# Kernel tuning notes

Hardware: AMD Instinct MI355X
Metric: run time of the kernel (lower is better)

## Reference

```python
import jax, jax.numpy as jnp
import numpy as np

N = 100000   # nodes
E = 3200000  # edges (avg degree 32)
K = 3        # num_stacks
L = 4        # num_layers (ARMA iterations)
H = 16       # hidden channels
C = 1        # num_classes
BN_EPS = 1e-5


def setup_inputs() -> dict:
    key = jax.random.key(0)
    ks = jax.random.split(key, 16)
    s = 0.1  # weight scale
    return {
        "x": jax.random.normal(ks[0], (N, 1), dtype=jnp.float32),
        "edge_index": jax.random.randint(ks[1], (2, E), 0, N, dtype=jnp.int64),
        "edge_attr": jax.random.uniform(ks[2], (E,), dtype=jnp.float32),
        "batch": jnp.zeros((N,), dtype=jnp.int64),
        # ARMAConv 1: 1 -> 16, shared weights
        "w1_init": s * jax.random.normal(ks[3], (K, 1, H), dtype=jnp.float32),
        "w1": s * jax.random.normal(ks[4], (K, H, H), dtype=jnp.float32),
        "w1_root": s * jax.random.normal(ks[5], (K, 1, H), dtype=jnp.float32),
        "b1": s * jax.random.normal(ks[6], (K, 1, H), dtype=jnp.float32),
        "bn1_g": jnp.ones((H,), dtype=jnp.float32),
        "bn1_b": jnp.zeros((H,), dtype=jnp.float32),
        # ARMAConv 2: 16 -> 1, shared weights, act=None
        "w2_init": s * jax.random.normal(ks[7], (K, H, C), dtype=jnp.float32),
        "w2": s * jax.random.normal(ks[8], (K, C, C), dtype=jnp.float32),
        "w2_root": s * jax.random.normal(ks[9], (K, H, C), dtype=jnp.float32),
        "b2": s * jax.random.normal(ks[10], (K, 1, C), dtype=jnp.float32),
    }


def _arma_conv(x, row, col, norm, w_init, w, w_root, b, n_layers, use_relu):
    """PyG ARMAConv with shared_weights=True, eval-mode dropout (identity).
    x: [N,Fin]; returns mean over K stacks: [N,Fout]."""
    n = x.shape[0]
    root = jnp.einsum('nf,kfo->kno', x, w_root)      # [K,N,Fout]
    out = jnp.einsum('nf,kfo->kno', x, w_init)       # [K,N,Fout]
    for t in range(n_layers):
        if t > 0:
            out = jnp.einsum('kno,kop->knp', out, w)
        # message: gather at source, scale by norm; aggregate (scatter-add) at target
        m = (out[:, row, :] * norm[None, :, None]).transpose(1, 0, 2)  # [E,K,F]
        out = jax.ops.segment_sum(m, col, num_segments=n).transpose(1, 0, 2)
        out = out + root + b
        if use_relu:
            out = jax.nn.relu(out)
    return out.mean(axis=0)


def reference(x, edge_index, edge_attr, batch, w1_init, w1, w1_root, b1,
              bn1_g, bn1_b, w2_init, w2, w2_root, b2):
    row, col = edge_index[0], edge_index[1]
    n = x.shape[0]
    # gcn_norm without self-loops: D^{-1/2} A D^{-1/2}
    deg = jax.ops.segment_sum(edge_attr, col, num_segments=n)
    dinv = jnp.where(deg > 0, jax.lax.rsqrt(jnp.maximum(deg, 1e-12)), 0.0)
    norm = dinv[row] * edge_attr * dinv[col]

    h = _arma_conv(x, row, col, norm, w1_init, w1, w1_root, b1, L, True)
    # BatchNorm1d (batch statistics) + ReLU; dropout is identity in eval
    mu = h.mean(axis=0)
    var = h.var(axis=0)
    h = (h - mu) * jax.lax.rsqrt(var + BN_EPS) * bn1_g + bn1_b
    h = jax.nn.relu(h)

    h = _arma_conv(h, row, col, norm, w2_init, w2, w2_root, b2, L, False)
    return jax.nn.sigmoid(h)
```

## Files before the change

### kernel.cpp

```cpp
#include <hip/hip_runtime.h>
#include <math.h>

#define N_NODES 100000
#define N_EDGES 3200000
#define KH 48
#define FDIM 64
#define NH 16
#define BN_EPS 1e-5f
#define NBUCK 196
#define BSHIFT 9
#define BMASK 511
#define EPB 16384
#define NBLK1 196
#define CAP 18432
#define FIX 16777216.0f

typedef unsigned long long u64;
typedef unsigned int u32;
typedef unsigned short u16;

__device__ __forceinline__ u16 f2bf(float f) {
  u32 b = __float_as_uint(f);
  b += 0x7FFFu + ((b >> 16) & 1u);
  return (u16)(b >> 16);
}
__device__ __forceinline__ float bf2f(u32 s) {
  return __uint_as_float(s << 16);
}
__device__ __forceinline__ u32 rfl(u32 v) {
  return (u32)__builtin_amdgcn_readfirstlane((int)v);
}

__global__ __launch_bounds__(1024) void bucket_scatter_kernel(
    const int* __restrict__ row, const int* __restrict__ col,
    const float* __restrict__ ea, u32* __restrict__ gcur,
    int2* __restrict__ bucketed) {
  __shared__ u32 bins[NBUCK];
  __shared__ u32 base[NBUCK];
  __shared__ u16 rnk[EPB];
  for (int t = threadIdx.x; t < NBUCK; t += 1024) bins[t] = 0;
  __syncthreads();
  int eb = blockIdx.x * EPB;
  for (int it = 0; it < EPB / 1024; ++it) {
    int i = it * 1024 + threadIdx.x;
    int e = eb + i;
    if (e < N_EDGES) rnk[i] = (u16)atomicAdd(&bins[col[e] >> BSHIFT], 1u);
  }
  __syncthreads();
  for (int t = threadIdx.x; t < NBUCK; t += 1024) {
    u32 c = bins[t];
    if (c) base[t] = (u32)t * CAP + atomicAdd(&gcur[t * 8], c);
  }
  __syncthreads();
  for (int it = 0; it < EPB / 1024; ++it) {
    int i = it * 1024 + threadIdx.x;
    int e = eb + i;
    if (e < N_EDGES) {
      int c = col[e];
      int bkt = c >> BSHIFT, cl = c & BMASK;
      u32 pos = base[bkt] + (u32)rnk[i];
      bucketed[pos] = make_int2((cl << 17) | row[e], __float_as_int(ea[e]));
    }
  }
}

__global__ __launch_bounds__(1024) void node_offs_csr_kernel(
    const int2* __restrict__ bucketed, const u32* __restrict__ gcur,
    const float* __restrict__ x,
    int* __restrict__ offs, float* __restrict__ dinv, u16* __restrict__ zx,
    u32* __restrict__ csr) {
  __shared__ u32 cnt[512];
  __shared__ u32 degf[512];
  __shared__ u32 cur[512];
  __shared__ u32 red[256];
  __shared__ u32 shmeta[2];
  int t = threadIdx.x;
  int b = blockIdx.x;
  if (t < 512) { cnt[t] = 0; degf[t] = 0; }
  if (t < 256) red[t] = (t < b) ? gcur[t * 8] : 0;
  __syncthreads();
  for (int d = 128; d; d >>= 1) {
    if (t < d) red[t] += red[t + d];
    __syncthreads();
  }
  if (t == 0) { shmeta[0] = red[0]; shmeta[1] = gcur[b * 8]; }
  __syncthreads();
  u32 bst = shmeta[0], fill = shmeta[1];
  u32 s_pad = (u32)b * CAP;
  for (u32 i = t; i < fill; i += 1024) {
    int2 v = bucketed[s_pad + i];
    int cl = (v.x >> 17) & BMASK;
    atomicAdd(&cnt[cl], 1u);
    atomicAdd(&degf[cl], (u32)(__int_as_float(v.y) * FIX));
  }
  __syncthreads();
  u32 v0 = (t < 512) ? cnt[t] : 0;
  for (int d = 1; d < 512; d <<= 1) {
    u32 u = (t < 512 && t >= d) ? cnt[t - d] : 0;
    __syncthreads();
    if (t < 512) cnt[t] += u;
    __syncthreads();
  }
  int n = b * 512 + t;
  if (t < 512) {
    if (n < N_NODES) {
      u32 off0 = bst + cnt[t] - v0;
      offs[n] = (int)off0;
      cur[t] = off0;
      float dg = (float)degf[t] * (1.0f / FIX);
      float dv = dg > 0.f ? rsqrtf(fmaxf(dg, 1e-12f)) : 0.f;
      dinv[n] = dv;
      zx[n] = f2bf(x[n] * dv);
    } else {
      cur[t] = 0;
    }
  }
  if (b == 0 && t == 0) offs[N_NODES] = N_EDGES;
  __syncthreads();
  for (u32 i = t; i < fill; i += 1024) {
    int2 v = bucketed[s_pad + i];
    int cl = (v.x >> 17) & BMASK;
    u32 r = (u32)(v.x & 0x1FFFF);
    u16 w = f2bf(__int_as_float(v.y));
    u32 pos = atomicAdd(&cur[cl], 1u);
    csr[pos] = (r << 15) | (u32)w;
  }
}

__global__ __launch_bounds__(256) void sprop_mid_kernel(
    const u32* __restrict__ csr, const int* __restrict__ offs,
    const u16* __restrict__ zx, const float* __restrict__ dinv,
    const float* __restrict__ x,
    const float* __restrict__ w1i, const float* __restrict__ w1r,
    const float* __restrict__ b1, const float* __restrict__ w1,
    u16* __restrict__ tout) {
  int t = blockIdx.x * 256 + threadIdx.x;
  int n = t >> 4, c = t & 15;
  float a = 0.f;
  int s = offs[n], e = offs[n + 1];
  for (int i = s + c; i < e; i += 16) {
    u32 ee = csr[i];
    a += bf2f(ee & 0x7FFFu) * bf2f((u32)zx[ee >> 15]);
  }
#pragma unroll
  for (int o = 8; o; o >>= 1) a += __shfl_xor(a, o, 64);
  float dn = dinv[n];
  float sn = a * dn;
  float xn = x[n];
  int base = (threadIdx.x & 63) & 48;
#pragma unroll
  for (int k = 0; k < 3; ++k) {
    float u = fmaxf(sn * w1i[k * 16 + c] + xn * w1r[k * 16 + c] + b1[k * 16 + c], 0.f);
    float tf = 0.f;
#pragma unroll
    for (int f = 0; f < 16; ++f) tf += __shfl(u, base + f, 64) * w1[k * 256 + f * 16 + c];
    tout[(size_t)n * FDIM + k * 16 + c] = f2bf(tf * dn);
  }
}

#define DECL16(p) u32 p##0, p##1, p##2, p##3, p##4, p##5, p##6, p##7, \
                      p##8, p##9, p##10, p##11, p##12, p##13, p##14, p##15
#define LOAD16(p, base) \
  p##0 = rfl(csr[(base)]);      p##1 = rfl(csr[(base) + 1]);  \
  p##2 = rfl(csr[(base) + 2]);  p##3 = rfl(csr[(base) + 3]);  \
  p##4 = rfl(csr[(base) + 4]);  p##5 = rfl(csr[(base) + 5]);  \
  p##6 = rfl(csr[(base) + 6]);  p##7 = rfl(csr[(base) + 7]);  \
  p##8 = rfl(csr[(base) + 8]);  p##9 = rfl(csr[(base) + 9]);  \
  p##10 = rfl(csr[(base) + 10]); p##11 = rfl(csr[(base) + 11]); \
  p##12 = rfl(csr[(base) + 12]); p##13 = rfl(csr[(base) + 13]); \
  p##14 = rfl(csr[(base) + 14]); p##15 = rfl(csr[(base) + 15])
#define COPY16(d, s2) \
  d##0 = s2##0; d##1 = s2##1; d##2 = s2##2; d##3 = s2##3; \
  d##4 = s2##4; d##5 = s2##5; d##6 = s2##6; d##7 = s2##7; \
  d##8 = s2##8; d##9 = s2##9; d##10 = s2##10; d##11 = s2##11; \
  d##12 = s2##12; d##13 = s2##13; d##14 = s2##14; d##15 = s2##15
#define PROC16(p) do { \
  float v0 = bf2f((u32)tin[(p##0 >> 15) * FDIM + c]); \
  float v1 = bf2f((u32)tin[(p##1 >> 15) * FDIM + c]); \
  float v2 = bf2f((u32)tin[(p##2 >> 15) * FDIM + c]); \
  float v3 = bf2f((u32)tin[(p##3 >> 15) * FDIM + c]); \
  float v4 = bf2f((u32)tin[(p##4 >> 15) * FDIM + c]); \
  float v5 = bf2f((u32)tin[(p##5 >> 15) * FDIM + c]); \
  float v6 = bf2f((u32)tin[(p##6 >> 15) * FDIM + c]); \
  float v7 = bf2f((u32)tin[(p##7 >> 15) * FDIM + c]); \
  float v8 = bf2f((u32)tin[(p##8 >> 15) * FDIM + c]); \
  float v9 = bf2f((u32)tin[(p##9 >> 15) * FDIM + c]); \
  float va = bf2f((u32)tin[(p##10 >> 15) * FDIM + c]); \
  float vb = bf2f((u32)tin[(p##11 >> 15) * FDIM + c]); \
  float vc = bf2f((u32)tin[(p##12 >> 15) * FDIM + c]); \
  float vd = bf2f((u32)tin[(p##13 >> 15) * FDIM + c]); \
  float ve = bf2f((u32)tin[(p##14 >> 15) * FDIM + c]); \
  float vf = bf2f((u32)tin[(p##15 >> 15) * FDIM + c]); \
  acc += bf2f(p##0 & 0x7FFFu) * v0 + bf2f(p##1 & 0x7FFFu) * v1 + \
         bf2f(p##2 & 0x7FFFu) * v2 + bf2f(p##3 & 0x7FFFu) * v3 + \
         bf2f(p##4 & 0x7FFFu) * v4 + bf2f(p##5 & 0x7FFFu) * v5 + \
         bf2f(p##6 & 0x7FFFu) * v6 + bf2f(p##7 & 0x7FFFu) * v7 + \
         bf2f(p##8 & 0x7FFFu) * v8 + bf2f(p##9 & 0x7FFFu) * v9 + \
         bf2f(p##10 & 0x7FFFu) * va + bf2f(p##11 & 0x7FFFu) * vb + \
         bf2f(p##12 & 0x7FFFu) * vc + bf2f(p##13 & 0x7FFFu) * vd + \
         bf2f(p##14 & 0x7FFFu) * ve + bf2f(p##15 & 0x7FFFu) * vf; \
} while (0)

__global__ __launch_bounds__(256) void conv1_prop_kernel(
    const u16* __restrict__ tin, u16* __restrict__ tout, float* __restrict__ hbuf,
    const u32* __restrict__ csr, const int* __restrict__ offs,
    const float* __restrict__ dinv, const float* __restrict__ x,
    const float* __restrict__ w1r, const float* __restrict__ b1,
    const float* __restrict__ w1, int do_t) {
  int lane = threadIdx.x & 63;
  int wid = (blockIdx.x * blockDim.x + threadIdx.x) >> 6;
  int nw = (gridDim.x * blockDim.x) >> 6;
  int c = lane;
  bool act = c < KH;
  float rb = act ? w1r[c] : 0.f;
  float bb = act ? b1[c] : 0.f;
  float wreg[16];
  if (do_t) {
    int k = c >> 4, o = c & 15;
    if (act) {
#pragma unroll
      for (int f = 0; f < 16; ++f) wreg[f] = w1[k * 256 + f * 16 + o];
    } else {
#pragma unroll
      for (int f = 0; f < 16; ++f) wreg[f] = 0.f;
    }
  }
  for (int n = wid; n < N_NODES; n += nw) {
    int nu = __builtin_amdgcn_readfirstlane(n);
    int s = __builtin_amdgcn_readfirstlane(offs[nu]);
    int e = __builtin_amdgcn_readfirstlane(offs[nu + 1]);
    float acc = 0.f;
    int i = s;
    int nblk = (e - s) >> 4;
    if (nblk > 0) {
      DECL16(a);
      DECL16(b);
      LOAD16(a, i);
      for (int blk = 1; blk < nblk; ++blk) {
        int j = i + 16;
        LOAD16(b, j);
        PROC16(a);
        COPY16(a, b);
        i = j;
      }
      PROC16(a);
      i += 16;
    }
    for (; i + 4 <= e; i += 4) {
      u32 e0 = rfl(csr[i]);
      u32 e1 = rfl(csr[i + 1]);
      u32 e2 = rfl(csr[i + 2]);
      u32 e3 = rfl(csr[i + 3]);
      float v0 = bf2f((u32)tin[(e0 >> 15) * FDIM + c]);
      float v1 = bf2f((u32)tin[(e1 >> 15) * FDIM + c]);
      float v2 = bf2f((u32)tin[(e2 >> 15) * FDIM + c]);
      float v3 = bf2f((u32)tin[(e3 >> 15) * FDIM + c]);
      acc += bf2f(e0 & 0x7FFFu) * v0 + bf2f(e1 & 0x7FFFu) * v1 +
             bf2f(e2 & 0x7FFFu) * v2 + bf2f(e3 & 0x7FFFu) * v3;
    }
    for (; i < e; ++i) {
      u32 ee = rfl(csr[i]);
      acc += bf2f(ee & 0x7FFFu) * bf2f((u32)tin[(ee >> 15) * FDIM + c]);
    }
    float dn = dinv[nu];
    float u = fmaxf(acc * dn + x[nu] * rb + bb, 0.f);
    if (do_t) {
      float tf = 0.f;
      int base = c & 48;
#pragma unroll
      for (int f = 0; f < 16; ++f) tf += __shfl(u, base + f, 64) * wreg[f];
      if (act) tout[(size_t)nu * FDIM + c] = f2bf(tf * dn);
    } else {
      float m1v = __shfl(u, lane + 16, 64);
      float m2v = __shfl(u, lane + 32, 64);
      if (lane < NH) hbuf[(size_t)nu * NH + lane] = (u + m1v + m2v) * (1.f / 3.f);
    }
  }
}

__global__ __launch_bounds__(256) void bn_stats_kernel(
    const float* __restrict__ h, double* __restrict__ stats) {
  __shared__ float ssum[NH], ssq[NH];
  int tid = threadIdx.x;
  if (tid < NH) { ssum[tid] = 0.f; ssq[tid] = 0.f; }
  __syncthreads();
  int n = blockIdx.x * blockDim.x + tid;
  bool valid = n < N_NODES;
  const float4* p = (const float4*)(h + (size_t)(valid ? n : 0) * NH);
  float hv[NH];
#pragma unroll
  for (int q = 0; q < 4; ++q) {
    float4 v = valid ? p[q] : make_float4(0.f, 0.f, 0.f, 0.f);
    hv[q * 4 + 0] = v.x; hv[q * 4 + 1] = v.y; hv[q * 4 + 2] = v.z; hv[q * 4 + 3] = v.w;
  }
#pragma unroll
  for (int f = 0; f < NH; ++f) {
    float s = hv[f], q = hv[f] * hv[f];
    for (int o = 32; o; o >>= 1) { s += __shfl_xor(s, o, 64); q += __shfl_xor(q, o, 64); }
    if ((tid & 63) == 0) { atomicAdd(&ssum[f], s); atomicAdd(&ssq[f], q); }
  }
  __syncthreads();
  if (tid < NH) {
    atomicAdd(&stats[tid], (double)ssum[tid]);
    atomicAdd(&stats[NH + tid], (double)ssq[tid]);
  }
}

__global__ __launch_bounds__(64) void bn_final_kernel(
    const double* __restrict__ stats, const float* __restrict__ g,
    const float* __restrict__ b, float* __restrict__ sc, float* __restrict__ sh) {
  int f = threadIdx.x;
  if (f < NH) {
    double mu = stats[f] / (double)N_NODES;
    double var = stats[NH + f] / (double)N_NODES - mu * mu;
    float scale = g[f] * (float)(1.0 / sqrt(var + (double)BN_EPS));
    sc[f] = scale;
    sh[f] = b[f] - (float)mu * scale;
  }
}

__global__ __launch_bounds__(256) void conv2_init_kernel(
    const float* __restrict__ h, const float* __restrict__ sc, const float* __restrict__ sh,
    const float* __restrict__ dinv,
    const float* __restrict__ w2i, const float* __restrict__ w2r, const float* __restrict__ b2,
    float* __restrict__ P, float* __restrict__ R) {
  int n = blockIdx.x * blockDim.x + threadIdx.x;
  if (n >= N_NODES) return;
  float u[NH];
#pragma unroll
  for (int f = 0; f < NH; ++f) u[f] = fmaxf(h[(size_t)n * NH + f] * sc[f] + sh[f], 0.f);
  float dn = dinv[n];
#pragma unroll
  for (int k = 0; k < 3; ++k) {
    float r = b2[k], o = 0.f;
#pragma unroll
    for (int f = 0; f < NH; ++f) {
      r += u[f] * w2r[k * NH + f];
      o += u[f] * w2i[k * NH + f];
    }
    R[n * 4 + k] = r;
    P[n * 4 + k] = o * dn;
  }
  R[n * 4 + 3] = 0.f;
  P[n * 4 + 3] = 0.f;
}

__global__ __launch_bounds__(256) void conv2_prop_kernel(
    const float* __restrict__ in4, float* __restrict__ out4, float* __restrict__ y,
    const u32* __restrict__ csr, const int* __restrict__ offs,
    const float* __restrict__ dinv,
    const float* __restrict__ R, const float* __restrict__ w2,
    int scale_w2, int final_out) {
  int t = blockIdx.x * 256 + threadIdx.x;
  int n = t >> 4, sub = t & 15;
  float m0 = 1.f, m1 = 1.f, m2 = 1.f;
  if (scale_w2) { m0 = w2[0]; m1 = w2[1]; m2 = w2[2]; }
  int s = offs[n], e = offs[n + 1];
  float a0 = 0.f, a1 = 0.f, a2 = 0.f;
  for (int i = s + sub; i < e; i += 16) {
    u32 ee = csr[i];
    float w = bf2f(ee & 0x7FFFu);
    const float4 v = *(const float4*)(in4 + (size_t)(ee >> 15) * 4);
    a0 += w * v.x;
    a1 += w * v.y;
    a2 += w * v.z;
  }
#pragma unroll
  for (int o = 8; o; o >>= 1) {
    a0 += __shfl_xor(a0, o, 64);
    a1 += __shfl_xor(a1, o, 64);
    a2 += __shfl_xor(a2, o, 64);
  }
  if (sub == 0) {
    float dn = dinv[n];
    a0 = a0 * dn * m0 + R[n * 4 + 0];
    a1 = a1 * dn * m1 + R[n * 4 + 1];
    a2 = a2 * dn * m2 + R[n * 4 + 2];
    if (final_out) {
      float sm = (a0 + a1 + a2) * (1.f / 3.f);
      y[n] = 1.f / (1.f + expf(-sm));
    } else {
      out4[n * 4 + 0] = a0 * dn;
      out4[n * 4 + 1] = a1 * dn;
      out4[n * 4 + 2] = a2 * dn;
      out4[n * 4 + 3] = 0.f;
    }
  }
}

extern "C" void kernel_launch(void* const* d_in, const int* in_sizes, int n_in,
                              void* d_out, int out_size, void* d_ws, size_t ws_size,
                              hipStream_t stream) {
  const float* x   = (const float*)d_in[0];
  const int*   ei  = (const int*)d_in[1];
  const float* ea  = (const float*)d_in[2];
  const float* w1i = (const float*)d_in[4];
  const float* w1  = (const float*)d_in[5];
  const float* w1r = (const float*)d_in[6];
  const float* b1  = (const float*)d_in[7];
  const float* bng = (const float*)d_in[8];
  const float* bnb = (const float*)d_in[9];
  const float* w2i = (const float*)d_in[10];
  const float* w2  = (const float*)d_in[11];
  const float* w2r = (const float*)d_in[12];
  const float* b2  = (const float*)d_in[13];
  float* y = (float*)d_out;

  const int* row = ei;
  const int* col = ei + N_EDGES;

  char* ws = (char*)d_ws;
  size_t off = 0;
  auto alloc = [&](size_t bytes) -> char* {
    char* p = ws + off;
    off += (bytes + 255) & ~(size_t)255;
    return p;
  };
  u32*    gcur   = (u32*)alloc((size_t)NBUCK * 8 * 4);
  int*    offs   = (int*)alloc((size_t)(N_NODES + 1) * 4);
  float*  dinv   = (float*)alloc((size_t)N_NODES * 4);
  u16*    zx     = (u16*)alloc((size_t)N_NODES * 2);
  double* stats  = (double*)alloc(32 * 8);
  float*  bnsc   = (float*)alloc(16 * 4);
  float*  bnsh   = (float*)alloc(16 * 4);
  int2*   bucketed = (int2*)alloc((size_t)NBUCK * CAP * 8);
  u32*    csr    = (u32*)alloc((size_t)N_EDGES * 4);
  u16*    tA     = (u16*)alloc((size_t)N_NODES * FDIM * 2);
  u16*    tB     = (u16*)alloc((size_t)N_NODES * FDIM * 2);
  float*  hbuf   = (float*)alloc((size_t)N_NODES * NH * 4);
  float*  P2     = (float*)alloc((size_t)N_NODES * 4 * 4);
  float*  Q2     = (float*)alloc((size_t)N_NODES * 4 * 4);
  float*  R2     = (float*)alloc((size_t)N_NODES * 4 * 4);
  (void)ws_size; (void)in_sizes; (void)n_in; (void)out_size;

  hipMemsetAsync(gcur, 0, (size_t)NBUCK * 8 * 4, stream);
  hipMemsetAsync(stats, 0, 32 * 8, stream);

  bucket_scatter_kernel<<<NBLK1, 1024, 0, stream>>>(row, col, ea, gcur, bucketed);
  node_offs_csr_kernel<<<NBUCK, 1024, 0, stream>>>(bucketed, gcur, x, offs, dinv, zx, csr);

  const int NPB = 6250;
  sprop_mid_kernel<<<NPB, 256, 0, stream>>>(csr, offs, zx, dinv, x, w1i, w1r, b1, w1, tA);
  conv1_prop_kernel<<<6250, 256, 0, stream>>>(tA, tB, nullptr, csr, offs, dinv, x, w1r, b1, w1, 1);
  conv1_prop_kernel<<<6250, 256, 0, stream>>>(tB, tA, nullptr, csr, offs, dinv, x, w1r, b1, w1, 1);
  conv1_prop_kernel<<<6250, 256, 0, stream>>>(tA, nullptr, hbuf, csr, offs, dinv, x, w1r, b1, w1, 0);

  bn_stats_kernel<<<(N_NODES + 255) / 256, 256, 0, stream>>>(hbuf, stats);
  bn_final_kernel<<<1, 64, 0, stream>>>(stats, bng, bnb, bnsc, bnsh);
  conv2_init_kernel<<<(N_NODES + 255) / 256, 256, 0, stream>>>(
      hbuf, bnsc, bnsh, dinv, w2i, w2r, b2, P2, R2);

  conv2_prop_kernel<<<NPB, 256, 0, stream>>>(P2, Q2, nullptr, csr, offs, dinv, R2, w2, 0, 0);
  conv2_prop_kernel<<<NPB, 256, 0, stream>>>(Q2, P2, nullptr, csr, offs, dinv, R2, w2, 1, 0);
  conv2_prop_kernel<<<NPB, 256, 0, stream>>>(P2, Q2, nullptr, csr, offs, dinv, R2, w2, 1, 0);
  conv2_prop_kernel<<<NPB, 256, 0, stream>>>(Q2, P2, y, csr, offs, dinv, R2, w2, 1, 1);
}
```

Baseline: 469.6 us.

## Software-pipeline CSR gathers two blocks deep and use nontemporal loads/stores

The conv1 propagation loop now issues the feature gathers for the next 16-edge block before doing the FMAs on the current block, alternating two register sets so more gather latency is in flight. Separately, CSR index loads and the output stores across the propagation kernels are marked nontemporal so that streaming data does not evict the gathered feature table from cache. The deeper pipelining raises register pressure, which may lower occupancy. The CSR array is re-read on every layer, so the nontemporal hint could make those repeat reads more expensive.

Measured after the change: 540.6 us. 1.15x slower.

```diff
diff --git a/kernel.cpp b/kernel.cpp
--- a/kernel.cpp
+++ b/kernel.cpp
@@ -139,7 +139,7 @@
   float a = 0.f;
   int s = offs[n], e = offs[n + 1];
   for (int i = s + c; i < e; i += 16) {
-    u32 ee = csr[i];
+    u32 ee = __builtin_nontemporal_load(csr + i);
     a += bf2f(ee & 0x7FFFu) * bf2f((u32)zx[ee >> 15]);
   }
 #pragma unroll
@@ -154,52 +154,55 @@
     float tf = 0.f;
 #pragma unroll
     for (int f = 0; f < 16; ++f) tf += __shfl(u, base + f, 64) * w1[k * 256 + f * 16 + c];
-    tout[(size_t)n * FDIM + k * 16 + c] = f2bf(tf * dn);
+    __builtin_nontemporal_store(f2bf(tf * dn), &tout[(size_t)n * FDIM + k * 16 + c]);
   }
 }
 
 #define DECL16(p) u32 p##0, p##1, p##2, p##3, p##4, p##5, p##6, p##7, \
                       p##8, p##9, p##10, p##11, p##12, p##13, p##14, p##15
 #define LOAD16(p, base) \
-  p##0 = rfl(csr[(base)]);      p##1 = rfl(csr[(base) + 1]);  \
-  p##2 = rfl(csr[(base) + 2]);  p##3 = rfl(csr[(base) + 3]);  \
-  p##4 = rfl(csr[(base) + 4]);  p##5 = rfl(csr[(base) + 5]);  \
-  p##6 = rfl(csr[(base) + 6]);  p##7 = rfl(csr[(base) + 7]);  \
-  p##8 = rfl(csr[(base) + 8]);  p##9 = rfl(csr[(base) + 9]);  \
-  p##10 = rfl(csr[(base) + 10]); p##11 = rfl(csr[(base) + 11]); \
-  p##12 = rfl(csr[(base) + 12]); p##13 = rfl(csr[(base) + 13]); \
-  p##14 = rfl(csr[(base) + 14]); p##15 = rfl(csr[(base) + 15])
-#define COPY16(d, s2) \
-  d##0 = s2##0; d##1 = s2##1; d##2 = s2##2; d##3 = s2##3; \
-  d##4 = s2##4; d##5 = s2##5; d##6 = s2##6; d##7 = s2##7; \
-  d##8 = s2##8; d##9 = s2##9; d##10 = s2##10; d##11 = s2##11; \
-  d##12 = s2##12; d##13 = s2##13; d##14 = s2##14; d##15 = s2##15
-#define PROC16(p) do { \
-  float v0 = bf2f((u32)tin[(p##0 >> 15) * FDIM + c]); \
-  float v1 = bf2f((u32)tin[(p##1 >> 15) * FDIM + c]); \
-  float v2 = bf2f((u32)tin[(p##2 >> 15) * FDIM + c]); \
-  float v3 = bf2f((u32)tin[(p##3 >> 15) * FDIM + c]); \
-  float v4 = bf2f((u32)tin[(p##4 >> 15) * FDIM + c]); \
-  float v5 = bf2f((u32)tin[(p##5 >> 15) * FDIM + c]); \
-  float v6 = bf2f((u32)tin[(p##6 >> 15) * FDIM + c]); \
-  float v7 = bf2f((u32)tin[(p##7 >> 15) * FDIM + c]); \
-  float v8 = bf2f((u32)tin[(p##8 >> 15) * FDIM + c]); \
-  float v9 = bf2f((u32)tin[(p##9 >> 15) * FDIM + c]); \
-  float va = bf2f((u32)tin[(p##10 >> 15) * FDIM + c]); \
-  float vb = bf2f((u32)tin[(p##11 >> 15) * FDIM + c]); \
-  float vc = bf2f((u32)tin[(p##12 >> 15) * FDIM + c]); \
-  float vd = bf2f((u32)tin[(p##13 >> 15) * FDIM + c]); \
-  float ve = bf2f((u32)tin[(p##14 >> 15) * FDIM + c]); \
-  float vf = bf2f((u32)tin[(p##15 >> 15) * FDIM + c]); \
-  acc += bf2f(p##0 & 0x7FFFu) * v0 + bf2f(p##1 & 0x7FFFu) * v1 + \
-         bf2f(p##2 & 0x7FFFu) * v2 + bf2f(p##3 & 0x7FFFu) * v3 + \
-         bf2f(p##4 & 0x7FFFu) * v4 + bf2f(p##5 & 0x7FFFu) * v5 + \
-         bf2f(p##6 & 0x7FFFu) * v6 + bf2f(p##7 & 0x7FFFu) * v7 + \
-         bf2f(p##8 & 0x7FFFu) * v8 + bf2f(p##9 & 0x7FFFu) * v9 + \
-         bf2f(p##10 & 0x7FFFu) * va + bf2f(p##11 & 0x7FFFu) * vb + \
-         bf2f(p##12 & 0x7FFFu) * vc + bf2f(p##13 & 0x7FFFu) * vd + \
-         bf2f(p##14 & 0x7FFFu) * ve + bf2f(p##15 & 0x7FFFu) * vf; \
-} while (0)
+  p##0 = rfl(__builtin_nontemporal_load(csr + (base)));      \
+  p##1 = rfl(__builtin_nontemporal_load(csr + (base) + 1));  \
+  p##2 = rfl(__builtin_nontemporal_load(csr + (base) + 2));  \
+  p##3 = rfl(__builtin_nontemporal_load(csr + (base) + 3));  \
+  p##4 = rfl(__builtin_nontemporal_load(csr + (base) + 4));  \
+  p##5 = rfl(__builtin_nontemporal_load(csr + (base) + 5));  \
+  p##6 = rfl(__builtin_nontemporal_load(csr + (base) + 6));  \
+  p##7 = rfl(__builtin_nontemporal_load(csr + (base) + 7));  \
+  p##8 = rfl(__builtin_nontemporal_load(csr + (base) + 8));  \
+  p##9 = rfl(__builtin_nontemporal_load(csr + (base) + 9));  \
+  p##10 = rfl(__builtin_nontemporal_load(csr + (base) + 10)); \
+  p##11 = rfl(__builtin_nontemporal_load(csr + (base) + 11)); \
+  p##12 = rfl(__builtin_nontemporal_load(csr + (base) + 12)); \
+  p##13 = rfl(__builtin_nontemporal_load(csr + (base) + 13)); \
+  p##14 = rfl(__builtin_nontemporal_load(csr + (base) + 14)); \
+  p##15 = rfl(__builtin_nontemporal_load(csr + (base) + 15))
+#define GATH16(g, p) \
+  g##0 = (u32)tin[(p##0 >> 15) * FDIM + c];  \
+  g##1 = (u32)tin[(p##1 >> 15) * FDIM + c];  \
+  g##2 = (u32)tin[(p##2 >> 15) * FDIM + c];  \
+  g##3 = (u32)tin[(p##3 >> 15) * FDIM + c];  \
+  g##4 = (u32)tin[(p##4 >> 15) * FDIM + c];  \
+  g##5 = (u32)tin[(p##5 >> 15) * FDIM + c];  \
+  g##6 = (u32)tin[(p##6 >> 15) * FDIM + c];  \
+  g##7 = (u32)tin[(p##7 >> 15) * FDIM + c];  \
+  g##8 = (u32)tin[(p##8 >> 15) * FDIM + c];  \
+  g##9 = (u32)tin[(p##9 >> 15) * FDIM + c];  \
+  g##10 = (u32)tin[(p##10 >> 15) * FDIM + c]; \
+  g##11 = (u32)tin[(p##11 >> 15) * FDIM + c]; \
+  g##12 = (u32)tin[(p##12 >> 15) * FDIM + c]; \
+  g##13 = (u32)tin[(p##13 >> 15) * FDIM + c]; \
+  g##14 = (u32)tin[(p##14 >> 15) * FDIM + c]; \
+  g##15 = (u32)tin[(p##15 >> 15) * FDIM + c]
+#define FMA16(p, g) \
+  acc += bf2f(p##0 & 0x7FFFu) * bf2f(g##0) + bf2f(p##1 & 0x7FFFu) * bf2f(g##1) + \
+         bf2f(p##2 & 0x7FFFu) * bf2f(g##2) + bf2f(p##3 & 0x7FFFu) * bf2f(g##3) + \
+         bf2f(p##4 & 0x7FFFu) * bf2f(g##4) + bf2f(p##5 & 0x7FFFu) * bf2f(g##5) + \
+         bf2f(p##6 & 0x7FFFu) * bf2f(g##6) + bf2f(p##7 & 0x7FFFu) * bf2f(g##7) + \
+         bf2f(p##8 & 0x7FFFu) * bf2f(g##8) + bf2f(p##9 & 0x7FFFu) * bf2f(g##9) + \
+         bf2f(p##10 & 0x7FFFu) * bf2f(g##10) + bf2f(p##11 & 0x7FFFu) * bf2f(g##11) + \
+         bf2f(p##12 & 0x7FFFu) * bf2f(g##12) + bf2f(p##13 & 0x7FFFu) * bf2f(g##13) + \
+         bf2f(p##14 & 0x7FFFu) * bf2f(g##14) + bf2f(p##15 & 0x7FFFu) * bf2f(g##15)
 
 __global__ __launch_bounds__(256) void conv1_prop_kernel(
     const u16* __restrict__ tin, u16* __restrict__ tout, float* __restrict__ hbuf,
@@ -235,22 +238,36 @@
     if (nblk > 0) {
       DECL16(a);
       DECL16(b);
+      DECL16(ga);
+      DECL16(gb);
       LOAD16(a, i);
-      for (int blk = 1; blk < nblk; ++blk) {
-        int j = i + 16;
-        LOAD16(b, j);
-        PROC16(a);
-        COPY16(a, b);
-        i = j;
+      GATH16(ga, a);
+      int blk = 1;
+      for (; blk + 1 < nblk; blk += 2) {
+        LOAD16(b, i + 16);
+        GATH16(gb, b);
+        FMA16(a, ga);
+        LOAD16(a, i + 32);
+        GATH16(ga, a);
+        FMA16(b, gb);
+        i += 32;
       }
-      PROC16(a);
-      i += 16;
+      if (blk < nblk) {
+        LOAD16(b, i + 16);
+        GATH16(gb, b);
+        FMA16(a, ga);
+        FMA16(b, gb);
+        i += 32;
+      } else {
+        FMA16(a, ga);
+        i += 16;
+      }
     }
     for (; i + 4 <= e; i += 4) {
-      u32 e0 = rfl(csr[i]);
-      u32 e1 = rfl(csr[i + 1]);
-      u32 e2 = rfl(csr[i + 2]);
-      u32 e3 = rfl(csr[i + 3]);
+      u32 e0 = rfl(__builtin_nontemporal_load(csr + i));
+      u32 e1 = rfl(__builtin_nontemporal_load(csr + i + 1));
+      u32 e2 = rfl(__builtin_nontemporal_load(csr + i + 2));
+      u32 e3 = rfl(__builtin_nontemporal_load(csr + i + 3));
       float v0 = bf2f((u32)tin[(e0 >> 15) * FDIM + c]);
       float v1 = bf2f((u32)tin[(e1 >> 15) * FDIM + c]);
       float v2 = bf2f((u32)tin[(e2 >> 15) * FDIM + c]);
@@ -259,7 +276,7 @@
              bf2f(e2 & 0x7FFFu) * v2 + bf2f(e3 & 0x7FFFu) * v3;
     }
     for (; i < e; ++i) {
-      u32 ee = rfl(csr[i]);
+      u32 ee = rfl(__builtin_nontemporal_load(csr + i));
       acc += bf2f(ee & 0x7FFFu) * bf2f((u32)tin[(ee >> 15) * FDIM + c]);
     }
     float dn = dinv[nu];
@@ -269,11 +286,13 @@
       int base = c & 48;
 #pragma unroll
       for (int f = 0; f < 16; ++f) tf += __shfl(u, base + f, 64) * wreg[f];
-      if (act) tout[(size_t)nu * FDIM + c] = f2bf(tf * dn);
+      if (act) __builtin_nontemporal_store(f2bf(tf * dn), &tout[(size_t)nu * FDIM + c]);
     } else {
       float m1v = __shfl(u, lane + 16, 64);
       float m2v = __shfl(u, lane + 32, 64);
-      if (lane < NH) hbuf[(size_t)nu * NH + lane] = (u + m1v + m2v) * (1.f / 3.f);
+      if (lane < NH)
+        __builtin_nontemporal_store((u + m1v + m2v) * (1.f / 3.f),
+                                    &hbuf[(size_t)nu * NH + lane]);
     }
   }
 }
@@ -358,7 +377,7 @@
   int s = offs[n], e = offs[n + 1];
   float a0 = 0.f, a1 = 0.f, a2 = 0.f;
   for (int i = s + sub; i < e; i += 16) {
-    u32 ee = csr[i];
+    u32 ee = __builtin_nontemporal_load(csr + i);
     float w = bf2f(ee & 0x7FFFu);
     const float4 v = *(const float4*)(in4 + (size_t)(ee >> 15) * 4);
     a0 += w * v.x;
```
